# Kernel tuning notes

Measured on AMD Instinct MI355X. Metric: run time of the kernel, lower is better.

Reference implementation:

```python
import jax, jax.numpy as jnp
import numpy as np

N = 100000
E = 1600000
IN_DIM, HID_DIM, OUT_DIM = 128, 128, 64


def setup_inputs() -> dict:
    key = jax.random.key(0)
    ks = jax.random.split(key, 8)
    x = jax.random.normal(ks[0], (N, IN_DIM), dtype=jnp.float32)
    edge_index = jax.random.randint(ks[1], (2, E), 0, N, dtype=jnp.int64)
    s = 1.0 / np.sqrt(IN_DIM)
    W1 = jax.random.normal(ks[2], (IN_DIM, HID_DIM), dtype=jnp.float32) * s
    Wd1 = jax.random.normal(ks[3], (IN_DIM, HID_DIM), dtype=jnp.float32) * s
    s2 = 1.0 / np.sqrt(HID_DIM)
    W2 = jax.random.normal(ks[4], (HID_DIM, OUT_DIM), dtype=jnp.float32) * s2
    Wd2 = jax.random.normal(ks[5], (HID_DIM, OUT_DIM), dtype=jnp.float32) * s2
    alpha1 = jnp.full((1,), 0.5, dtype=jnp.float32)
    beta1 = jnp.full((1,), 0.5, dtype=jnp.float32)
    alpha2 = jnp.full((1,), 0.5, dtype=jnp.float32)
    beta2 = jnp.full((1,), 0.5, dtype=jnp.float32)
    return dict(x=x, edge_index=edge_index, W1=W1, Wd1=Wd1, alpha1=alpha1,
                beta1=beta1, W2=W2, Wd2=Wd2, alpha2=alpha2, beta2=beta2)


def _edge_weights(row, col, num_nodes, dtype):
    # D_out^{-1/2} A D_in^{-1/2} expressed per-edge
    ones = jnp.ones(row.shape[0], dtype=dtype)
    deg_out = jax.ops.segment_sum(ones, row, num_segments=num_nodes)
    deg_in = jax.ops.segment_sum(ones, col, num_segments=num_nodes)
    inv_sqrt = lambda d: jnp.where(d > 0, jax.lax.rsqrt(jnp.maximum(d, 1.0)), 0.0)
    return inv_sqrt(deg_out)[row] * inv_sqrt(deg_in)[col]


def _dir_conv(x, row, col, edge_w, num_nodes, W, Wd, alpha, beta):
    transformed = x @ W                       # [N, out]
    msg = transformed[col] * edge_w[:, None]  # gather + scale, [E, out]
    h_base = jax.ops.segment_sum(msg, row, num_segments=num_nodes)
    h_dir = alpha * transformed + beta * (x @ Wd)
    return h_base + h_dir


def reference(x, edge_index, W1, Wd1, alpha1, beta1, W2, Wd2, alpha2, beta2):
    row, col = edge_index[0], edge_index[1]
    num_nodes = x.shape[0]
    edge_w = _edge_weights(row, col, num_nodes, x.dtype)
    h = _dir_conv(x, row, col, edge_w, num_nodes, W1, Wd1, alpha1, beta1)
    h = jax.nn.relu(h)
    # dropout is identity in eval mode
    out = _dir_conv(h, row, col, edge_w, num_nodes, W2, Wd2, alpha2, beta2)
    return out
```

## Files before the change

kernel.cpp:

```cpp
#include <hip/hip_runtime.h>

#define N_NODES 100000
#define N_EDGES 1600000
#define ELL_W   64

typedef __attribute__((ext_vector_type(8))) short bf16x8;
typedef __attribute__((ext_vector_type(4))) float f32x4;

__device__ __forceinline__ unsigned short rne16(float x) {
    unsigned u = __float_as_uint(x);
    u += 0x7fffu + ((u >> 16) & 1u);
    return (unsigned short)(u >> 16);
}
__device__ __forceinline__ float bf16_lo(unsigned u) { return __uint_as_float(u << 16); }
__device__ __forceinline__ float bf16_hi(unsigned u) { return __uint_as_float(u & 0xffff0000u); }

__global__ __launch_bounds__(256) void build_ell(const int* __restrict__ ei,
                                                 unsigned* __restrict__ cnt_out,
                                                 unsigned* __restrict__ cnt_in,
                                                 int* __restrict__ ell) {
    int e = blockIdx.x * 256 + threadIdx.x;
    if (e >= N_EDGES) return;
    int r = ei[e];
    int c = ei[N_EDGES + e];
    unsigned pos = atomicAdd(&cnt_out[r], 1u);
    if (pos < ELL_W) ell[(size_t)r * ELL_W + pos] = c;
    atomicAdd(&cnt_in[c], 1u);
}

__global__ __launch_bounds__(256) void dinv_kernel(const unsigned* __restrict__ deg_out,
                                                   const unsigned* __restrict__ deg_in,
                                                   float* __restrict__ dinv_out,
                                                   float* __restrict__ dinv_in) {
    int n = blockIdx.x * 256 + threadIdx.x;
    if (n >= N_NODES) return;
    unsigned d0 = deg_out[n];
    unsigned d1 = deg_in[n];
    dinv_out[n] = d0 ? rsqrtf((float)d0) : 0.0f;
    dinv_in[n]  = d1 ? rsqrtf((float)d1) : 0.0f;
}

__global__ __launch_bounds__(256) void wprep(const float* __restrict__ W, int Mcols,
                                             unsigned short* __restrict__ Wh,
                                             unsigned short* __restrict__ Wl) {
    int idx = blockIdx.x * 256 + threadIdx.x;
    if (idx >= 128 * Mcols) return;
    int m = idx % Mcols, k = idx / Mcols;
    float w = W[idx];
    unsigned short h = rne16(w);
    float hf = __uint_as_float((unsigned)h << 16);
    unsigned short l = rne16(w - hf);
    Wh[m * 128 + k] = h;
    Wl[m * 128 + k] = l;
}

template <int M>
__global__ __launch_bounds__(256) void gemm_mfma(const float* __restrict__ A,
                                                 const unsigned short* __restrict__ Wah,
                                                 const unsigned short* __restrict__ Wal,
                                                 const unsigned short* __restrict__ Wbh,
                                                 const unsigned short* __restrict__ Wbl,
                                                 const float* __restrict__ alpha,
                                                 const float* __restrict__ beta,
                                                 unsigned short* __restrict__ Tb,
                                                 float* __restrict__ Hd) {
    constexpr int NI = M / 64;
    __shared__ unsigned short sH[64 * 128];
    __shared__ unsigned short sL[64 * 128];

    const int tid = threadIdx.x;
    const int w = tid >> 6;
    const int lane = tid & 63;
    const int rowBase = blockIdx.x * 64;

    #pragma unroll
    for (int it = 0; it < 8; ++it) {
        int flat = it * 256 + tid;
        int r = flat >> 5, c4 = flat & 31;
        int gr = rowBase + r;
        float4 v = make_float4(0.f, 0.f, 0.f, 0.f);
        if (gr < N_NODES) v = *(const float4*)&A[(size_t)gr * 128 + c4 * 4];
        unsigned short hx = rne16(v.x), hy = rne16(v.y), hz = rne16(v.z), hw = rne16(v.w);
        float lx = v.x - __uint_as_float((unsigned)hx << 16);
        float ly = v.y - __uint_as_float((unsigned)hy << 16);
        float lz = v.z - __uint_as_float((unsigned)hz << 16);
        float lw = v.w - __uint_as_float((unsigned)hw << 16);
        uint2 hi2, lo2;
        hi2.x = (unsigned)hx | ((unsigned)hy << 16);
        hi2.y = (unsigned)hz | ((unsigned)hw << 16);
        lo2.x = (unsigned)rne16(lx) | ((unsigned)rne16(ly) << 16);
        lo2.y = (unsigned)rne16(lz) | ((unsigned)rne16(lw) << 16);
        unsigned byte = (unsigned)(r * 256 + c4 * 8) ^ ((unsigned)(r & 7) << 4);
        *(uint2*)((char*)sH + byte) = hi2;
        *(uint2*)((char*)sL + byte) = lo2;
    }
    __syncthreads();

    const int colBase = w * (16 * NI);
    const int g  = lane >> 4;
    const int ln = lane & 15;
    const unsigned swz = ((unsigned)(ln & 7)) << 4;

    f32x4 acc[2][4][NI] = {};

    #pragma unroll
    for (int ks = 0; ks < 4; ++ks) {
        bf16x8 ah[4], al[4];
        #pragma unroll
        for (int mi = 0; mi < 4; ++mi) {
            unsigned byte = ((unsigned)((mi * 16 + ln) * 256 + ks * 64 + g * 16)) ^ swz;
            ah[mi] = *(const bf16x8*)((const char*)sH + byte);
            al[mi] = *(const bf16x8*)((const char*)sL + byte);
        }
        #pragma unroll
        for (int mat = 0; mat < 2; ++mat) {
            const unsigned short* __restrict__ Wh = mat ? Wbh : Wah;
            const unsigned short* __restrict__ Wl = mat ? Wbl : Wal;
            #pragma unroll
            for (int ni = 0; ni < NI; ++ni) {
                int col = colBase + ni * 16 + ln;
                size_t off = (size_t)col * 128 + ks * 32 + g * 8;
                bf16x8 wh = *(const bf16x8*)&Wh[off];
                bf16x8 wl = *(const bf16x8*)&Wl[off];
                #pragma unroll
                for (int mi = 0; mi < 4; ++mi) {
                    acc[mat][mi][ni] = __builtin_amdgcn_mfma_f32_16x16x32_bf16(ah[mi], wh, acc[mat][mi][ni], 0, 0, 0);
                    acc[mat][mi][ni] = __builtin_amdgcn_mfma_f32_16x16x32_bf16(al[mi], wh, acc[mat][mi][ni], 0, 0, 0);
                    acc[mat][mi][ni] = __builtin_amdgcn_mfma_f32_16x16x32_bf16(ah[mi], wl, acc[mat][mi][ni], 0, 0, 0);
                }
            }
        }
    }

    const float al_ = alpha[0], be_ = beta[0];
    #pragma unroll
    for (int mi = 0; mi < 4; ++mi) {
        #pragma unroll
        for (int ni = 0; ni < NI; ++ni) {
            #pragma unroll
            for (int r = 0; r < 4; ++r) {
                int row = rowBase + mi * 16 + g * 4 + r;
                if (row >= N_NODES) continue;
                int col = colBase + ni * 16 + ln;
                float t = acc[0][mi][ni][r];
                float d = fmaf(al_, t, be_ * acc[1][mi][ni][r]);
                Tb[(size_t)row * M + col] = rne16(t);
                Hd[(size_t)row * M + col] = d;
            }
        }
    }
}

__global__ __launch_bounds__(256) void agg_kernel_128(const unsigned* __restrict__ deg,
                                                      const int* __restrict__ ell,
                                                      const float* __restrict__ dinv_out,
                                                      const float* __restrict__ dinv_in,
                                                      const unsigned* __restrict__ Tb,
                                                      float* __restrict__ H) {
    int node = blockIdx.x * 4 + (threadIdx.x >> 6);
    if (node >= N_NODES) return;
    int lane = threadIdx.x & 63;
    unsigned d = deg[node];
    if (d > ELL_W) d = ELL_W;
    const int* __restrict__ cl = &ell[(size_t)node * ELL_W];
    float dn = dinv_out[node];
    float2* __restrict__ Hv = (float2*)H;
    float2 acc = Hv[(size_t)node * 64 + lane];
    unsigned i = 0;
    for (; i + 4 <= d; i += 4) {
        int c0 = cl[i], c1 = cl[i + 1], c2 = cl[i + 2], c3 = cl[i + 3];
        float w0 = dn * dinv_in[c0];
        float w1 = dn * dinv_in[c1];
        float w2 = dn * dinv_in[c2];
        float w3 = dn * dinv_in[c3];
        unsigned u0 = Tb[(size_t)c0 * 64 + lane];
        unsigned u1 = Tb[(size_t)c1 * 64 + lane];
        unsigned u2 = Tb[(size_t)c2 * 64 + lane];
        unsigned u3 = Tb[(size_t)c3 * 64 + lane];
        acc.x = fmaf(w0, bf16_lo(u0), acc.x); acc.y = fmaf(w0, bf16_hi(u0), acc.y);
        acc.x = fmaf(w1, bf16_lo(u1), acc.x); acc.y = fmaf(w1, bf16_hi(u1), acc.y);
        acc.x = fmaf(w2, bf16_lo(u2), acc.x); acc.y = fmaf(w2, bf16_hi(u2), acc.y);
        acc.x = fmaf(w3, bf16_lo(u3), acc.x); acc.y = fmaf(w3, bf16_hi(u3), acc.y);
    }
    for (; i < d; ++i) {
        int c0 = cl[i];
        float w0 = dn * dinv_in[c0];
        unsigned u0 = Tb[(size_t)c0 * 64 + lane];
        acc.x = fmaf(w0, bf16_lo(u0), acc.x); acc.y = fmaf(w0, bf16_hi(u0), acc.y);
    }
    acc.x = fmaxf(acc.x, 0.0f);
    acc.y = fmaxf(acc.y, 0.0f);
    Hv[(size_t)node * 64 + lane] = acc;
}

__global__ __launch_bounds__(256) void agg_kernel_64(const unsigned* __restrict__ deg,
                                                     const int* __restrict__ ell,
                                                     const float* __restrict__ dinv_out,
                                                     const float* __restrict__ dinv_in,
                                                     const unsigned short* __restrict__ Tb,
                                                     float* __restrict__ Out) {
    int node = blockIdx.x * 4 + (threadIdx.x >> 6);
    if (node >= N_NODES) return;
    int lane = threadIdx.x & 63;
    unsigned d = deg[node];
    if (d > ELL_W) d = ELL_W;
    const int* __restrict__ cl = &ell[(size_t)node * ELL_W];
    float dn = dinv_out[node];
    float acc = Out[(size_t)node * 64 + lane];
    unsigned i = 0;
    for (; i + 4 <= d; i += 4) {
        int c0 = cl[i], c1 = cl[i + 1], c2 = cl[i + 2], c3 = cl[i + 3];
        float w0 = dn * dinv_in[c0];
        float w1 = dn * dinv_in[c1];
        float w2 = dn * dinv_in[c2];
        float w3 = dn * dinv_in[c3];
        float t0 = __uint_as_float(((unsigned)Tb[(size_t)c0 * 64 + lane]) << 16);
        float t1 = __uint_as_float(((unsigned)Tb[(size_t)c1 * 64 + lane]) << 16);
        float t2 = __uint_as_float(((unsigned)Tb[(size_t)c2 * 64 + lane]) << 16);
        float t3 = __uint_as_float(((unsigned)Tb[(size_t)c3 * 64 + lane]) << 16);
        acc = fmaf(w0, t0, acc);
        acc = fmaf(w1, t1, acc);
        acc = fmaf(w2, t2, acc);
        acc = fmaf(w3, t3, acc);
    }
    for (; i < d; ++i) {
        int c0 = cl[i];
        float t0 = __uint_as_float(((unsigned)Tb[(size_t)c0 * 64 + lane]) << 16);
        acc = fmaf(dn * dinv_in[c0], t0, acc);
    }
    Out[(size_t)node * 64 + lane] = acc;
}

extern "C" void kernel_launch(void* const* d_in, const int* in_sizes, int n_in,
                              void* d_out, int out_size, void* d_ws, size_t ws_size,
                              hipStream_t stream) {
    const float* x   = (const float*)d_in[0];
    const int*   ei  = (const int*)d_in[1];
    const float* W1  = (const float*)d_in[2];
    const float* Wd1 = (const float*)d_in[3];
    const float* a1  = (const float*)d_in[4];
    const float* b1  = (const float*)d_in[5];
    const float* W2  = (const float*)d_in[6];
    const float* Wd2 = (const float*)d_in[7];
    const float* a2  = (const float*)d_in[8];
    const float* b2  = (const float*)d_in[9];
    float* out = (float*)d_out;

    char* ws = (char*)d_ws;
    size_t off = 0;
    auto alloc = [&](size_t bytes) -> void* {
        void* p = ws + off;
        off = (off + bytes + 255) & ~(size_t)255;
        return p;
    };

    unsigned* cnt_out = (unsigned*)alloc(2 * sizeof(unsigned) * N_NODES);
    unsigned* cnt_in  = cnt_out + N_NODES;
    float* dinv_out   = (float*)alloc(sizeof(float) * N_NODES);
    float* dinv_in    = (float*)alloc(sizeof(float) * N_NODES);
    int* ell          = (int*)alloc(sizeof(int) * (size_t)N_NODES * ELL_W);
    unsigned* T1      = (unsigned*)alloc(sizeof(unsigned) * (size_t)N_NODES * 64);
    float* H1         = (float*)alloc(sizeof(float) * (size_t)N_NODES * 128);
    unsigned* T2      = (unsigned*)alloc(sizeof(unsigned) * (size_t)N_NODES * 32);
    unsigned short* wt1a_h = (unsigned short*)alloc(sizeof(short) * 128 * 128);
    unsigned short* wt1a_l = (unsigned short*)alloc(sizeof(short) * 128 * 128);
    unsigned short* wt1b_h = (unsigned short*)alloc(sizeof(short) * 128 * 128);
    unsigned short* wt1b_l = (unsigned short*)alloc(sizeof(short) * 128 * 128);
    unsigned short* wt2a_h = (unsigned short*)alloc(sizeof(short) * 64 * 128);
    unsigned short* wt2a_l = (unsigned short*)alloc(sizeof(short) * 64 * 128);
    unsigned short* wt2b_h = (unsigned short*)alloc(sizeof(short) * 64 * 128);
    unsigned short* wt2b_l = (unsigned short*)alloc(sizeof(short) * 64 * 128);

    (void)hipMemsetAsync(cnt_out, 0, 2 * sizeof(unsigned) * N_NODES, stream);

    wprep<<<64, 256, 0, stream>>>(W1,  128, wt1a_h, wt1a_l);
    wprep<<<64, 256, 0, stream>>>(Wd1, 128, wt1b_h, wt1b_l);
    wprep<<<32, 256, 0, stream>>>(W2,   64, wt2a_h, wt2a_l);
    wprep<<<32, 256, 0, stream>>>(Wd2,  64, wt2b_h, wt2b_l);

    build_ell<<<(N_EDGES + 255) / 256, 256, 0, stream>>>(ei, cnt_out, cnt_in, ell);
    dinv_kernel<<<(N_NODES + 255) / 256, 256, 0, stream>>>(cnt_out, cnt_in, dinv_out, dinv_in);

    const int gblocks = (N_NODES + 63) / 64;

    gemm_mfma<128><<<gblocks, 256, 0, stream>>>(x, wt1a_h, wt1a_l, wt1b_h, wt1b_l, a1, b1,
                                                (unsigned short*)T1, H1);
    agg_kernel_128<<<(N_NODES + 3) / 4, 256, 0, stream>>>(cnt_out, ell, dinv_out, dinv_in, T1, H1);

    gemm_mfma<64><<<gblocks, 256, 0, stream>>>(H1, wt2a_h, wt2a_l, wt2b_h, wt2b_l, a2, b2,
                                               (unsigned short*)T2, out);
    agg_kernel_64<<<(N_NODES + 3) / 4, 256, 0, stream>>>(cnt_out, ell, dinv_out, dinv_in,
                                                         (const unsigned short*)T2, out);
}
```

Baseline: 388.3 us.

## Merge prep launches, co-schedule ELL build with GEMM1, prescale layer-2 features by dinv_in

Folds the four weight-prep launches and the counter memset into one prep kernel. Runs the edge-to-ELL build and the first GEMM as disjoint block ranges of a single launch so the atomic-heavy build can overlap with the MFMA work. Layer-2 features are multiplied by dinv_in inside the second GEMM epilogue, so the layer-2 aggregation no longer gathers dinv_in per neighbor and applies dinv_out once at the end. In exchange the bf16 rounding now happens after scaling, the fused launch has uneven block types, and the edge blocks drop their bounds check because E divides evenly by 256.

```diff
diff --git a/kernel.cpp b/kernel.cpp
--- a/kernel.cpp
+++ b/kernel.cpp
@@ -3,6 +3,7 @@
 #define N_NODES 100000
 #define N_EDGES 1600000
 #define ELL_W   64
+#define EB      6250
 
 typedef __attribute__((ext_vector_type(8))) short bf16x8;
 typedef __attribute__((ext_vector_type(4))) float f32x4;
@@ -15,17 +16,32 @@
 __device__ __forceinline__ float bf16_lo(unsigned u) { return __uint_as_float(u << 16); }
 __device__ __forceinline__ float bf16_hi(unsigned u) { return __uint_as_float(u & 0xffff0000u); }
 
-__global__ __launch_bounds__(256) void build_ell(const int* __restrict__ ei,
-                                                 unsigned* __restrict__ cnt_out,
-                                                 unsigned* __restrict__ cnt_in,
-                                                 int* __restrict__ ell) {
-    int e = blockIdx.x * 256 + threadIdx.x;
-    if (e >= N_EDGES) return;
-    int r = ei[e];
-    int c = ei[N_EDGES + e];
-    unsigned pos = atomicAdd(&cnt_out[r], 1u);
-    if (pos < ELL_W) ell[(size_t)r * ELL_W + pos] = c;
-    atomicAdd(&cnt_in[c], 1u);
+__device__ __forceinline__ void wprep_elem(const float* __restrict__ W, int Mcols, int idx,
+                                           unsigned short* __restrict__ Wh,
+                                           unsigned short* __restrict__ Wl) {
+    int m = idx % Mcols, k = idx / Mcols;
+    float w = W[idx];
+    unsigned short h = rne16(w);
+    float hf = __uint_as_float((unsigned)h << 16);
+    Wh[m * 128 + k] = h;
+    Wl[m * 128 + k] = rne16(w - hf);
+}
+
+__global__ __launch_bounds__(256) void prep_kernel(const float* __restrict__ W1,
+                                                   const float* __restrict__ Wd1,
+                                                   const float* __restrict__ W2,
+                                                   const float* __restrict__ Wd2,
+                                                   unsigned short* __restrict__ w1h, unsigned short* __restrict__ w1l,
+                                                   unsigned short* __restrict__ wd1h, unsigned short* __restrict__ wd1l,
+                                                   unsigned short* __restrict__ w2h, unsigned short* __restrict__ w2l,
+                                                   unsigned short* __restrict__ wd2h, unsigned short* __restrict__ wd2l,
+                                                   unsigned* __restrict__ cnt) {
+    int i = blockIdx.x * 256 + threadIdx.x;
+    if (i < 16384)            wprep_elem(W1, 128, i, w1h, w1l);
+    else if (i < 32768)       wprep_elem(Wd1, 128, i - 16384, wd1h, wd1l);
+    else if (i < 40960)       wprep_elem(W2, 64, i - 32768, w2h, w2l);
+    else if (i < 49152)       wprep_elem(Wd2, 64, i - 40960, wd2h, wd2l);
+    else if (i < 49152 + 2 * N_NODES) cnt[i - 49152] = 0u;
 }
 
 __global__ __launch_bounds__(256) void dinv_kernel(const unsigned* __restrict__ deg_out,
@@ -40,30 +56,18 @@
     dinv_in[n]  = d1 ? rsqrtf((float)d1) : 0.0f;
 }
 
-__global__ __launch_bounds__(256) void wprep(const float* __restrict__ W, int Mcols,
-                                             unsigned short* __restrict__ Wh,
-                                             unsigned short* __restrict__ Wl) {
-    int idx = blockIdx.x * 256 + threadIdx.x;
-    if (idx >= 128 * Mcols) return;
-    int m = idx % Mcols, k = idx / Mcols;
-    float w = W[idx];
-    unsigned short h = rne16(w);
-    float hf = __uint_as_float((unsigned)h << 16);
-    unsigned short l = rne16(w - hf);
-    Wh[m * 128 + k] = h;
-    Wl[m * 128 + k] = l;
-}
-
-template <int M>
-__global__ __launch_bounds__(256) void gemm_mfma(const float* __restrict__ A,
-                                                 const unsigned short* __restrict__ Wah,
-                                                 const unsigned short* __restrict__ Wal,
-                                                 const unsigned short* __restrict__ Wbh,
-                                                 const unsigned short* __restrict__ Wbl,
-                                                 const float* __restrict__ alpha,
-                                                 const float* __restrict__ beta,
-                                                 unsigned short* __restrict__ Tb,
-                                                 float* __restrict__ Hd) {
+template <int M, bool SCALE_T>
+__device__ __forceinline__ void gemm_body(const float* __restrict__ A,
+                                          const unsigned short* __restrict__ Wah,
+                                          const unsigned short* __restrict__ Wal,
+                                          const unsigned short* __restrict__ Wbh,
+                                          const unsigned short* __restrict__ Wbl,
+                                          const float* __restrict__ alpha,
+                                          const float* __restrict__ beta,
+                                          const float* __restrict__ dinv_in,
+                                          unsigned short* __restrict__ Tb,
+                                          float* __restrict__ Hd,
+                                          int bid) {
     constexpr int NI = M / 64;
     __shared__ unsigned short sH[64 * 128];
     __shared__ unsigned short sL[64 * 128];
@@ -71,7 +75,7 @@
     const int tid = threadIdx.x;
     const int w = tid >> 6;
     const int lane = tid & 63;
-    const int rowBase = blockIdx.x * 64;
+    const int rowBase = bid * 64;
 
     #pragma unroll
     for (int it = 0; it < 8; ++it) {
@@ -144,11 +148,50 @@
                 int col = colBase + ni * 16 + ln;
                 float t = acc[0][mi][ni][r];
                 float d = fmaf(al_, t, be_ * acc[1][mi][ni][r]);
-                Tb[(size_t)row * M + col] = rne16(t);
+                float ts = SCALE_T ? dinv_in[row] * t : t;
+                Tb[(size_t)row * M + col] = rne16(ts);
                 Hd[(size_t)row * M + col] = d;
             }
         }
     }
+}
+
+__global__ __launch_bounds__(256) void build_and_gemm1(const int* __restrict__ ei,
+                                                       unsigned* __restrict__ cnt_out,
+                                                       unsigned* __restrict__ cnt_in,
+                                                       int* __restrict__ ell,
+                                                       const float* __restrict__ x,
+                                                       const unsigned short* __restrict__ Wah,
+                                                       const unsigned short* __restrict__ Wal,
+                                                       const unsigned short* __restrict__ Wbh,
+                                                       const unsigned short* __restrict__ Wbl,
+                                                       const float* __restrict__ alpha,
+                                                       const float* __restrict__ beta,
+                                                       unsigned short* __restrict__ Tb,
+                                                       float* __restrict__ Hd) {
+    if (blockIdx.x < EB) {
+        int e = blockIdx.x * 256 + threadIdx.x;
+        int r = ei[e];
+        int c = ei[N_EDGES + e];
+        unsigned pos = atomicAdd(&cnt_out[r], 1u);
+        if (pos < ELL_W) ell[(size_t)r * ELL_W + pos] = c;
+        atomicAdd(&cnt_in[c], 1u);
+    } else {
+        gemm_body<128, false>(x, Wah, Wal, Wbh, Wbl, alpha, beta, nullptr, Tb, Hd, blockIdx.x - EB);
+    }
+}
+
+__global__ __launch_bounds__(256) void gemm2_kernel(const float* __restrict__ A,
+                                                    const unsigned short* __restrict__ Wah,
+                                                    const unsigned short* __restrict__ Wal,
+                                                    const unsigned short* __restrict__ Wbh,
+                                                    const unsigned short* __restrict__ Wbl,
+                                                    const float* __restrict__ alpha,
+                                                    const float* __restrict__ beta,
+                                                    const float* __restrict__ dinv_in,
+                                                    unsigned short* __restrict__ Tb,
+                                                    float* __restrict__ Hd) {
+    gemm_body<64, true>(A, Wah, Wal, Wbh, Wbl, alpha, beta, dinv_in, Tb, Hd, blockIdx.x);
 }
 
 __global__ __launch_bounds__(256) void agg_kernel_128(const unsigned* __restrict__ deg,
@@ -196,7 +239,6 @@
 __global__ __launch_bounds__(256) void agg_kernel_64(const unsigned* __restrict__ deg,
                                                      const int* __restrict__ ell,
                                                      const float* __restrict__ dinv_out,
-                                                     const float* __restrict__ dinv_in,
                                                      const unsigned short* __restrict__ Tb,
                                                      float* __restrict__ Out) {
     int node = blockIdx.x * 4 + (threadIdx.x >> 6);
@@ -206,29 +248,21 @@
     if (d > ELL_W) d = ELL_W;
     const int* __restrict__ cl = &ell[(size_t)node * ELL_W];
     float dn = dinv_out[node];
-    float acc = Out[(size_t)node * 64 + lane];
+    float acc = 0.0f;
     unsigned i = 0;
     for (; i + 4 <= d; i += 4) {
         int c0 = cl[i], c1 = cl[i + 1], c2 = cl[i + 2], c3 = cl[i + 3];
-        float w0 = dn * dinv_in[c0];
-        float w1 = dn * dinv_in[c1];
-        float w2 = dn * dinv_in[c2];
-        float w3 = dn * dinv_in[c3];
         float t0 = __uint_as_float(((unsigned)Tb[(size_t)c0 * 64 + lane]) << 16);
         float t1 = __uint_as_float(((unsigned)Tb[(size_t)c1 * 64 + lane]) << 16);
         float t2 = __uint_as_float(((unsigned)Tb[(size_t)c2 * 64 + lane]) << 16);
         float t3 = __uint_as_float(((unsigned)Tb[(size_t)c3 * 64 + lane]) << 16);
-        acc = fmaf(w0, t0, acc);
-        acc = fmaf(w1, t1, acc);
-        acc = fmaf(w2, t2, acc);
-        acc = fmaf(w3, t3, acc);
+        acc += t0 + t1;
+        acc += t2 + t3;
     }
     for (; i < d; ++i) {
-        int c0 = cl[i];
-        float t0 = __uint_as_float(((unsigned)Tb[(size_t)c0 * 64 + lane]) << 16);
-        acc = fmaf(dn * dinv_in[c0], t0, acc);
-    }
-    Out[(size_t)node * 64 + lane] = acc;
+        acc += __uint_as_float(((unsigned)Tb[(size_t)cl[i] * 64 + lane]) << 16);
+    }
+    Out[(size_t)node * 64 + lane] = fmaf(dn, acc, Out[(size_t)node * 64 + lane]);
 }
 
 extern "C" void kernel_launch(void* const* d_in, const int* in_sizes, int n_in,
@@ -271,24 +305,23 @@
     unsigned short* wt2b_h = (unsigned short*)alloc(sizeof(short) * 64 * 128);
     unsigned short* wt2b_l = (unsigned short*)alloc(sizeof(short) * 64 * 128);
 
-    (void)hipMemsetAsync(cnt_out, 0, 2 * sizeof(unsigned) * N_NODES, stream);
-
-    wprep<<<64, 256, 0, stream>>>(W1,  128, wt1a_h, wt1a_l);
-    wprep<<<64, 256, 0, stream>>>(Wd1, 128, wt1b_h, wt1b_l);
-    wprep<<<32, 256, 0, stream>>>(W2,   64, wt2a_h, wt2a_l);
-    wprep<<<32, 256, 0, stream>>>(Wd2,  64, wt2b_h, wt2b_l);
-
-    build_ell<<<(N_EDGES + 255) / 256, 256, 0, stream>>>(ei, cnt_out, cnt_in, ell);
+    const int prep_total = 49152 + 2 * N_NODES;
+    prep_kernel<<<(prep_total + 255) / 256, 256, 0, stream>>>(
+        W1, Wd1, W2, Wd2, wt1a_h, wt1a_l, wt1b_h, wt1b_l,
+        wt2a_h, wt2a_l, wt2b_h, wt2b_l, cnt_out);
+
+    const int gblocks = (N_NODES + 63) / 64;
+
+    build_and_gemm1<<<EB + gblocks, 256, 0, stream>>>(ei, cnt_out, cnt_in, ell,
+                                                      x, wt1a_h, wt1a_l, wt1b_h, wt1b_l,
+                                                      a1, b1, (unsigned short*)T1, H1);
+
     dinv_kernel<<<(N_NODES + 255) / 256, 256, 0, stream>>>(cnt_out, cnt_in, dinv_out, dinv_in);
 
-    const int gblocks = (N_NODES + 63) / 64;
-
-    gemm_mfma<128><<<gblocks, 256, 0, stream>>>(x, wt1a_h, wt1a_l, wt1b_h, wt1b_l, a1, b1,
-                                                (unsigned short*)T1, H1);
     agg_kernel_128<<<(N_NODES + 3) / 4, 256, 0, stream>>>(cnt_out, ell, dinv_out, dinv_in, T1, H1);
 
-    gemm_mfma<64><<<gblocks, 256, 0, stream>>>(H1, wt2a_h, wt2a_l, wt2b_h, wt2b_l, a2, b2,
-                                               (unsigned short*)T2, out);
-    agg_kernel_64<<<(N_NODES + 3) / 4, 256, 0, stream>>>(cnt_out, ell, dinv_out, dinv_in,
+    gemm2_kernel<<<gblocks, 256, 0, stream>>>(H1, wt2a_h, wt2a_l, wt2b_h, wt2b_l, a2, b2,
+                                              dinv_in, (unsigned short*)T2, out);
+    agg_kernel_64<<<(N_NODES + 3) / 4, 256, 0, stream>>>(cnt_out, ell, dinv_out,
                                                          (const unsigned short*)T2, out);
 }
```

Result: no change. 381.5 us (-1.8%).
